# Performance work log

Measured on AMD Instinct MI355X. Metric: run time of the kernel, lower is better.

Reference implementation:

```python
import jax, jax.numpy as jnp
import numpy as np

N_NODES = 100000
N_EDGES = 1600000
EMB = 64
H1 = 128
H2 = 64


def gcn_conv(x, edge_index, W, b, num_nodes):
    # PyG GCNConv: x' = D^{-1/2}(A+I)D^{-1/2} (x W) + b, with self-loops
    x = x @ W  # [N, out]
    src, dst = edge_index[0], edge_index[1]
    loop = jnp.arange(num_nodes, dtype=src.dtype)
    src_f = jnp.concatenate([src, loop])
    dst_f = jnp.concatenate([dst, loop])
    deg = jax.ops.segment_sum(jnp.ones_like(src_f, dtype=x.dtype), dst_f,
                              num_segments=num_nodes)
    dinv = jnp.where(deg > 0, jax.lax.rsqrt(deg), 0.0)
    norm = dinv[src_f] * dinv[dst_f]           # [E+N]
    msg = x[src_f] * norm[:, None]             # gather + scale
    out = jax.ops.segment_sum(msg, dst_f, num_segments=num_nodes)
    return out + b


def setup_inputs() -> dict:
    key = jax.random.key(0)
    ks = jax.random.split(key, 12)
    category_ids = jax.random.randint(ks[0], (N_NODES,), 0, 1000)
    sub_category_ids = jax.random.randint(ks[1], (N_NODES,), 0, 5000)
    element_ids = jax.random.randint(ks[2], (N_NODES,), 0, 100000)
    edge_index = jax.random.randint(ks[3], (2, N_EDGES), 0, N_NODES)
    cat_table = jax.random.normal(ks[4], (1000, EMB), dtype=jnp.float32)
    sub_table = jax.random.normal(ks[5], (5000, EMB), dtype=jnp.float32)
    elem_table = jax.random.normal(ks[6], (100000, EMB), dtype=jnp.float32)
    W1 = jax.random.normal(ks[7], (3 * EMB, H1), dtype=jnp.float32) * (1.0 / np.sqrt(3 * EMB))
    b1 = jnp.zeros((H1,), dtype=jnp.float32)
    W2 = jax.random.normal(ks[8], (H1, H2), dtype=jnp.float32) * (1.0 / np.sqrt(H1))
    b2 = jnp.zeros((H2,), dtype=jnp.float32)
    return {
        "category_ids": category_ids,
        "sub_category_ids": sub_category_ids,
        "element_ids": element_ids,
        "edge_index": edge_index,
        "cat_table": cat_table,
        "sub_table": sub_table,
        "elem_table": elem_table,
        "W1": W1, "b1": b1, "W2": W2, "b2": b2,
    }


def reference(category_ids, sub_category_ids, element_ids, edge_index,
              cat_table, sub_table, elem_table, W1, b1, W2, b2):
    # NodeEmbedding: concat of three 64-dim lookups -> [N, 192]
    x = jnp.concatenate([cat_table[category_ids],
                         sub_table[sub_category_ids],
                         elem_table[element_ids]], axis=-1)
    x = jax.nn.relu(gcn_conv(x, edge_index, W1, b1, N_NODES))
    # dropout(0.3) is identity in eval mode
    x = jax.nn.relu(gcn_conv(x, edge_index, W2, b2, N_NODES))
    return x
```

## Files before the change

### kernel.cpp

```cpp
#include <hip/hip_runtime.h>

#define N_NODES 100000
#define EMB     64
#define H1      128
#define H2      64

#define BSHIFT  7
#define NBUCK   782
#define CAP     3072

#define OFF_DINV  0
#define OFF_ROWP  100004
#define OFF_COL   200008
#define OFF_GFILL 1800008
#define OFF_GBASE 1800792
#define OFF_SCR   1801576
#define OFF_H     4203880
#define OFF_Y     10603880
#define OFF_PCAT  17003880
#define OFF_PSUB  17131880

static __device__ __forceinline__ unsigned short f2bf(float f) {
    unsigned int u = __float_as_uint(f);
    unsigned int r = (u + 0x7fffu + ((u >> 16) & 1u)) >> 16;
    return (unsigned short)r;
}
static __device__ __forceinline__ unsigned int pack2bf(float a, float b) {
    return (unsigned int)f2bf(a) | ((unsigned int)f2bf(b) << 16);
}
static __device__ __forceinline__ float bflo(unsigned int u) {
    return __uint_as_float(u << 16);
}
static __device__ __forceinline__ float bfhi(unsigned int u) {
    return __uint_as_float(u & 0xffff0000u);
}


__global__ __launch_bounds__(256) void k_bin(
    const int* __restrict__ src, const int* __restrict__ dst, int E,
    int* __restrict__ gfill, unsigned int* __restrict__ scr)
{
    __shared__ int hist[NBUCK];
    __shared__ int basec[NBUCK];
    int t = threadIdx.x;
    for (int i = t; i < NBUCK; i += 256) hist[i] = 0;
    __syncthreads();
    int chunk = (E + gridDim.x - 1) / gridDim.x;
    int e0 = blockIdx.x * chunk;
    int e1 = min(e0 + chunk, E);
    for (int i = e0 + t; i < e1; i += 256)
        atomicAdd(&hist[dst[i] >> BSHIFT], 1);
    __syncthreads();
    for (int b = t; b < NBUCK; b += 256) {
        int c = hist[b];
        basec[b] = (c > 0) ? atomicAdd(&gfill[b], c) : 0;
        hist[b] = 0;
    }
    __syncthreads();
    for (int i = e0 + t; i < e1; i += 256) {
        int d = dst[i];
        int b = d >> BSHIFT;
        int slot = basec[b] + atomicAdd(&hist[b], 1);
        if (slot < CAP)
            scr[(size_t)b * CAP + slot] =
                ((unsigned int)(d & 127) << 17) | (unsigned int)src[i];
    }
}


__global__ __launch_bounds__(256) void k_bscan(
    const int* __restrict__ gfill, int* __restrict__ gbase,
    int* __restrict__ rowp, int E)
{
    __shared__ int sh[256];
    int t = threadIdx.x;
    int v[4]; int s = 0;
    #pragma unroll
    for (int u = 0; u < 4; ++u) {
        int i = t * 4 + u;
        v[u] = (i < NBUCK) ? gfill[i] : 0;
        s += v[u];
    }
    sh[t] = s;
    __syncthreads();
    for (int off = 1; off < 256; off <<= 1) {
        int x = (t >= off) ? sh[t - off] : 0;
        __syncthreads();
        sh[t] += x;
        __syncthreads();
    }
    int run = (t == 0) ? 0 : sh[t - 1];
    #pragma unroll
    for (int u = 0; u < 4; ++u) {
        int i = t * 4 + u;
        if (i < NBUCK) gbase[i] = run;
        run += v[u];
    }
    if (t == 255) { gbase[NBUCK] = run; rowp[N_NODES] = E; }
}


__global__ __launch_bounds__(256) void k_csr(
    const unsigned int* __restrict__ scr, const int* __restrict__ gfill,
    const int* __restrict__ gbase, int N,
    int* __restrict__ rowp, int* __restrict__ col, float* __restrict__ dinv)
{
    __shared__ unsigned int stage[CAP];
    __shared__ int hist[128];
    __shared__ int offs[128];
    __shared__ int cur[128];
    int b = blockIdx.x, t = threadIdx.x;
    int cnt = gfill[b];
    if (cnt > CAP) cnt = CAP;
    int base = gbase[b];
    if (t < 128) hist[t] = 0;
    __syncthreads();
    for (int i = t; i < cnt; i += 256) {
        unsigned int p = scr[(size_t)b * CAP + i];
        stage[i] = p;
        atomicAdd(&hist[p >> 17], 1);
    }
    __syncthreads();
    if (t < 128) offs[t] = hist[t];
    __syncthreads();
    for (int off = 1; off < 128; off <<= 1) {
        int x = 0;
        if (t < 128 && t >= off) x = offs[t - off];
        __syncthreads();
        if (t < 128) offs[t] += x;
        __syncthreads();
    }
    if (t < 128) {
        int excl = offs[t] - hist[t];
        cur[t] = 0;
        int d = b * 128 + t;
        if (d < N) {
            rowp[d] = base + excl;
            dinv[d] = rsqrtf((float)(hist[t] + 1));
        }
        offs[t] = excl;
    }
    __syncthreads();
    for (int i = t; i < cnt; i += 256) {
        unsigned int p = stage[i];
        int dl = (int)(p >> 17);
        int pos = offs[dl] + atomicAdd(&cur[dl], 1);
        col[base + pos] = (int)(p & 0x1FFFFu);
    }
}


__global__ __launch_bounds__(256) void k_ptab(
    const float* __restrict__ tab, const float* __restrict__ Wseg,
    float* __restrict__ P, int R)
{
    __shared__ float Wl[64][128];
    int t = threadIdx.x;
    for (int idx = t; idx < 64 * 128; idx += 256)
        Wl[idx >> 7][idx & 127] = Wseg[idx];
    __syncthreads();
    int cg = t & 31, ng = t >> 5;
    int r = blockIdx.x * 8 + ng;
    if (r >= R) return;
    const float* x = tab + (size_t)r * 64;
    float4 acc = make_float4(0.f, 0.f, 0.f, 0.f);
    #pragma unroll 8
    for (int k = 0; k < 64; ++k) {
        float xx = x[k];
        float4 w = *(const float4*)&Wl[k][cg * 4];
        acc.x += xx * w.x; acc.y += xx * w.y;
        acc.z += xx * w.z; acc.w += xx * w.w;
    }
    *(float4*)&P[(size_t)r * 128 + cg * 4] = acc;
}


__global__ __launch_bounds__(256) void k_gemm1(
    const int* __restrict__ cid, const int* __restrict__ sid, const int* __restrict__ eid,
    const float* __restrict__ elem_t, const float* __restrict__ W1,
    const float* __restrict__ Pcat, const float* __restrict__ Psub,
    const float* __restrict__ dinv,
    unsigned short* __restrict__ hb, int N)
{
    __shared__ float Wl[64][128];
    int t = threadIdx.x;
    const float* Wc = W1 + 128 * 128;
    for (int idx = t; idx < 64 * 128; idx += 256)
        Wl[idx >> 7][idx & 127] = Wc[idx];
    __syncthreads();

    int cg = t & 31;
    int ng = t >> 5;
    int n0 = blockIdx.x << 6;

    const float* rp[8];
    #pragma unroll
    for (int i = 0; i < 8; ++i) {
        int n = n0 + ng + 8 * i;
        int id = eid[(n < N) ? n : 0];
        rp[i] = elem_t + (size_t)id * 64;
    }
    float4 acc[8];
    #pragma unroll
    for (int i = 0; i < 8; ++i) acc[i] = make_float4(0.f, 0.f, 0.f, 0.f);

    #pragma unroll 4
    for (int k4 = 0; k4 < 16; ++k4) {
        float4 xv[8];
        #pragma unroll
        for (int i = 0; i < 8; ++i)
            xv[i] = *(const float4*)(rp[i] + k4 * 4);
        #pragma unroll
        for (int kk = 0; kk < 4; ++kk) {
            float4 w = *(const float4*)&Wl[k4 * 4 + kk][cg * 4];
            #pragma unroll
            for (int i = 0; i < 8; ++i) {
                float xx = (kk == 0) ? xv[i].x : (kk == 1) ? xv[i].y
                         : (kk == 2) ? xv[i].z : xv[i].w;
                acc[i].x += xx * w.x;
                acc[i].y += xx * w.y;
                acc[i].z += xx * w.z;
                acc[i].w += xx * w.w;
            }
        }
    }
    #pragma unroll
    for (int i = 0; i < 8; ++i) {
        int n = n0 + ng + 8 * i;
        if (n < N) {
            float4 pc = *(const float4*)&Pcat[(size_t)cid[n] * 128 + cg * 4];
            float4 ps = *(const float4*)&Psub[(size_t)sid[n] * 128 + cg * 4];
            float s = dinv[n];
            uint2 p;
            p.x = pack2bf((acc[i].x + pc.x + ps.x) * s, (acc[i].y + pc.y + ps.y) * s);
            p.y = pack2bf((acc[i].z + pc.z + ps.z) * s, (acc[i].w + pc.w + ps.w) * s);
            *(uint2*)(hb + (size_t)n * 128 + cg * 4) = p;
        }
    }
}


__global__ __launch_bounds__(256) void k_gemm2(
    const unsigned int* __restrict__ yb, const float* __restrict__ W2,
    const float* __restrict__ dinv,
    unsigned short* __restrict__ h2b, int N)
{
    __shared__ float Wl[128][64];
    int t = threadIdx.x;
    for (int idx = t; idx < 128 * 64; idx += 256)
        Wl[idx >> 6][idx & 63] = W2[idx];
    __syncthreads();

    int cg = t & 15;
    int ng = t >> 4;
    int n0 = blockIdx.x << 7;
    const unsigned int* rp[8];
    float4 acc[8];
    #pragma unroll
    for (int i = 0; i < 8; ++i) {
        acc[i] = make_float4(0.f, 0.f, 0.f, 0.f);
        int n = n0 + ng + 16 * i;
        rp[i] = yb + (size_t)((n < N) ? n : (N - 1)) * 64;
    }
    #pragma unroll 4
    for (int k4 = 0; k4 < 32; ++k4) {
        uint2 xv[8];
        #pragma unroll
        for (int i = 0; i < 8; ++i)
            xv[i] = *(const uint2*)(rp[i] + k4 * 2);
        #pragma unroll
        for (int kk = 0; kk < 4; ++kk) {
            float4 w = *(const float4*)&Wl[k4 * 4 + kk][cg * 4];
            #pragma unroll
            for (int i = 0; i < 8; ++i) {
                float xx = (kk == 0) ? bflo(xv[i].x) : (kk == 1) ? bfhi(xv[i].x)
                         : (kk == 2) ? bflo(xv[i].y) : bfhi(xv[i].y);
                acc[i].x += xx * w.x;
                acc[i].y += xx * w.y;
                acc[i].z += xx * w.z;
                acc[i].w += xx * w.w;
            }
        }
    }
    #pragma unroll
    for (int i = 0; i < 8; ++i) {
        int n = n0 + ng + 16 * i;
        if (n < N) {
            float s = dinv[n];
            uint2 p;
            p.x = pack2bf(acc[i].x * s, acc[i].y * s);
            p.y = pack2bf(acc[i].z * s, acc[i].w * s);
            *(uint2*)(h2b + (size_t)n * 64 + cg * 4) = p;
        }
    }
}


__global__ __launch_bounds__(256) void k_agg1(
    const unsigned short* __restrict__ hb, const int* __restrict__ rowp,
    const int* __restrict__ col, const float* __restrict__ dinv,
    const float* __restrict__ b1, unsigned int* __restrict__ yb, int N)
{
    int wv = threadIdx.x >> 6;
    int lane = threadIdx.x & 63;
    int d = blockIdx.x * 4 + wv;
    if (d >= N) return;
    const unsigned int* hp = (const unsigned int*)hb;
    float dd = dinv[d];
    unsigned int su = hp[(size_t)d * 64 + lane];
    float ax0 = bflo(su), ay0 = bfhi(su);
    float ax1 = 0.f, ay1 = 0.f, ax2 = 0.f, ay2 = 0.f, ax3 = 0.f, ay3 = 0.f;
    float ax4 = 0.f, ay4 = 0.f, ax5 = 0.f, ay5 = 0.f, ax6 = 0.f, ay6 = 0.f;
    float ax7 = 0.f, ay7 = 0.f;
    int e = rowp[d], e1 = rowp[d + 1];
    for (; e + 8 <= e1; e += 8) {
        int s0 = col[e + 0], s1 = col[e + 1], s2 = col[e + 2], s3 = col[e + 3];
        int s4 = col[e + 4], s5 = col[e + 5], s6 = col[e + 6], s7 = col[e + 7];
        unsigned int u0 = hp[(size_t)s0 * 64 + lane];
        unsigned int u1 = hp[(size_t)s1 * 64 + lane];
        unsigned int u2 = hp[(size_t)s2 * 64 + lane];
        unsigned int u3 = hp[(size_t)s3 * 64 + lane];
        unsigned int u4 = hp[(size_t)s4 * 64 + lane];
        unsigned int u5 = hp[(size_t)s5 * 64 + lane];
        unsigned int u6 = hp[(size_t)s6 * 64 + lane];
        unsigned int u7 = hp[(size_t)s7 * 64 + lane];
        ax0 += bflo(u0); ay0 += bfhi(u0);
        ax1 += bflo(u1); ay1 += bfhi(u1);
        ax2 += bflo(u2); ay2 += bfhi(u2);
        ax3 += bflo(u3); ay3 += bfhi(u3);
        ax4 += bflo(u4); ay4 += bfhi(u4);
        ax5 += bflo(u5); ay5 += bfhi(u5);
        ax6 += bflo(u6); ay6 += bfhi(u6);
        ax7 += bflo(u7); ay7 += bfhi(u7);
    }
    for (; e < e1; ++e) {
        unsigned int u = hp[(size_t)col[e] * 64 + lane];
        ax0 += bflo(u); ay0 += bfhi(u);
    }
    float2 bb = *(const float2*)&b1[lane * 2];
    float rx = dd * (((ax0 + ax1) + (ax2 + ax3)) + ((ax4 + ax5) + (ax6 + ax7))) + bb.x;
    float ry = dd * (((ay0 + ay1) + (ay2 + ay3)) + ((ay4 + ay5) + (ay6 + ay7))) + bb.y;
    yb[(size_t)d * 64 + lane] = pack2bf(rx > 0.f ? rx : 0.f, ry > 0.f ? ry : 0.f);
}


__global__ __launch_bounds__(256) void k_agg2(
    const unsigned short* __restrict__ h2b, const int* __restrict__ rowp,
    const int* __restrict__ col, const float* __restrict__ dinv,
    const float* __restrict__ b2, float* __restrict__ out, int N)
{
    int wv = threadIdx.x >> 6;
    int lane = threadIdx.x & 63;
    int d = blockIdx.x * 4 + wv;
    if (d >= N) return;
    float dd = dinv[d];
    float a0 = __uint_as_float((unsigned int)h2b[(size_t)d * 64 + lane] << 16);
    float a1 = 0.f, a2 = 0.f, a3 = 0.f, a4 = 0.f, a5 = 0.f, a6 = 0.f, a7 = 0.f;
    int e = rowp[d], e1 = rowp[d + 1];
    for (; e + 8 <= e1; e += 8) {
        int s0 = col[e + 0], s1 = col[e + 1], s2 = col[e + 2], s3 = col[e + 3];
        int s4 = col[e + 4], s5 = col[e + 5], s6 = col[e + 6], s7 = col[e + 7];
        a0 += __uint_as_float((unsigned int)h2b[(size_t)s0 * 64 + lane] << 16);
        a1 += __uint_as_float((unsigned int)h2b[(size_t)s1 * 64 + lane] << 16);
        a2 += __uint_as_float((unsigned int)h2b[(size_t)s2 * 64 + lane] << 16);
        a3 += __uint_as_float((unsigned int)h2b[(size_t)s3 * 64 + lane] << 16);
        a4 += __uint_as_float((unsigned int)h2b[(size_t)s4 * 64 + lane] << 16);
        a5 += __uint_as_float((unsigned int)h2b[(size_t)s5 * 64 + lane] << 16);
        a6 += __uint_as_float((unsigned int)h2b[(size_t)s6 * 64 + lane] << 16);
        a7 += __uint_as_float((unsigned int)h2b[(size_t)s7 * 64 + lane] << 16);
    }
    for (; e < e1; ++e)
        a0 += __uint_as_float((unsigned int)h2b[(size_t)col[e] * 64 + lane] << 16);
    float v = dd * (((a0 + a1) + (a2 + a3)) + ((a4 + a5) + (a6 + a7))) + b2[lane];
    out[(size_t)d * 64 + lane] = v > 0.f ? v : 0.f;
}


extern "C" void kernel_launch(void* const* d_in, const int* in_sizes, int n_in,
                              void* d_out, int out_size, void* d_ws, size_t ws_size,
                              hipStream_t stream) {
    const int*   cid    = (const int*)d_in[0];
    const int*   sid    = (const int*)d_in[1];
    const int*   eid    = (const int*)d_in[2];
    const int*   edge   = (const int*)d_in[3];
    const float* cat_t  = (const float*)d_in[4];
    const float* sub_t  = (const float*)d_in[5];
    const float* elem_t = (const float*)d_in[6];
    const float* W1     = (const float*)d_in[7];
    const float* b1     = (const float*)d_in[8];
    const float* W2     = (const float*)d_in[9];
    const float* b2     = (const float*)d_in[10];
    float* out = (float*)d_out;

    int N = in_sizes[0];
    int E = in_sizes[3] / 2;
    const int* src = edge;
    const int* dst = edge + E;

    int*   ws    = (int*)d_ws;
    float* dinv  = (float*)(ws + OFF_DINV);
    int*   rowp  = ws + OFF_ROWP;
    int*   col   = ws + OFF_COL;
    int*   gfill = ws + OFF_GFILL;
    int*   gbase = ws + OFF_GBASE;
    unsigned int* scr = (unsigned int*)(ws + OFF_SCR);
    unsigned short* hb = (unsigned short*)(ws + OFF_H);
    unsigned int*   yb = (unsigned int*)(ws + OFF_Y);
    float* Pcat = (float*)(ws + OFF_PCAT);
    float* Psub = (float*)(ws + OFF_PSUB);

    hipMemsetAsync(gfill, 0, NBUCK * sizeof(int), stream);

    k_ptab<<<125, 256, 0, stream>>>(cat_t, W1,            Pcat, 1000);
    k_ptab<<<625, 256, 0, stream>>>(sub_t, W1 + 64 * 128, Psub, 5000);

    k_bin<<<200, 256, 0, stream>>>(src, dst, E, gfill, scr);
    k_bscan<<<1, 256, 0, stream>>>(gfill, gbase, rowp, E);
    k_csr<<<NBUCK, 256, 0, stream>>>(scr, gfill, gbase, N, rowp, col, dinv);

    k_gemm1<<<(N + 63) / 64, 256, 0, stream>>>(cid, sid, eid, elem_t, W1, Pcat, Psub, dinv, hb, N);
    k_agg1<<<(N + 3) / 4, 256, 0, stream>>>(hb, rowp, col, dinv, b1, yb, N);
    k_gemm2<<<(N + 127) / 128, 256, 0, stream>>>(yb, W2, dinv, hb, N);
    k_agg2<<<(N + 3) / 4, 256, 0, stream>>>(hb, rowp, col, dinv, b2, out, N);
}
```

Measured before the change: 429.0 us.

## Process two destination nodes per wavefront in aggregation and enlarge CSR-build blocks

```diff
diff --git a/kernel.cpp b/kernel.cpp
--- a/kernel.cpp
+++ b/kernel.cpp
@@ -36,28 +36,28 @@
 }
 
 
-__global__ __launch_bounds__(256) void k_bin(
+__global__ __launch_bounds__(1024) void k_bin(
     const int* __restrict__ src, const int* __restrict__ dst, int E,
     int* __restrict__ gfill, unsigned int* __restrict__ scr)
 {
     __shared__ int hist[NBUCK];
     __shared__ int basec[NBUCK];
     int t = threadIdx.x;
-    for (int i = t; i < NBUCK; i += 256) hist[i] = 0;
+    for (int i = t; i < NBUCK; i += 1024) hist[i] = 0;
     __syncthreads();
     int chunk = (E + gridDim.x - 1) / gridDim.x;
     int e0 = blockIdx.x * chunk;
     int e1 = min(e0 + chunk, E);
-    for (int i = e0 + t; i < e1; i += 256)
+    for (int i = e0 + t; i < e1; i += 1024)
         atomicAdd(&hist[dst[i] >> BSHIFT], 1);
     __syncthreads();
-    for (int b = t; b < NBUCK; b += 256) {
+    for (int b = t; b < NBUCK; b += 1024) {
         int c = hist[b];
         basec[b] = (c > 0) ? atomicAdd(&gfill[b], c) : 0;
         hist[b] = 0;
     }
     __syncthreads();
-    for (int i = e0 + t; i < e1; i += 256) {
+    for (int i = e0 + t; i < e1; i += 1024) {
         int d = dst[i];
         int b = d >> BSHIFT;
         int slot = basec[b] + atomicAdd(&hist[b], 1);
@@ -100,7 +100,7 @@
 }
 
 
-__global__ __launch_bounds__(256) void k_csr(
+__global__ __launch_bounds__(512) void k_csr(
     const unsigned int* __restrict__ scr, const int* __restrict__ gfill,
     const int* __restrict__ gbase, int N,
     int* __restrict__ rowp, int* __restrict__ col, float* __restrict__ dinv)
@@ -115,7 +115,7 @@
     int base = gbase[b];
     if (t < 128) hist[t] = 0;
     __syncthreads();
-    for (int i = t; i < cnt; i += 256) {
+    for (int i = t; i < cnt; i += 512) {
         unsigned int p = scr[(size_t)b * CAP + i];
         stage[i] = p;
         atomicAdd(&hist[p >> 17], 1);
@@ -141,7 +141,7 @@
         offs[t] = excl;
     }
     __syncthreads();
-    for (int i = t; i < cnt; i += 256) {
+    for (int i = t; i < cnt; i += 512) {
         unsigned int p = stage[i];
         int dl = (int)(p >> 17);
         int pos = offs[dl] + atomicAdd(&cur[dl], 1);
@@ -299,80 +299,128 @@
 __global__ __launch_bounds__(256) void k_agg1(
     const unsigned short* __restrict__ hb, const int* __restrict__ rowp,
     const int* __restrict__ col, const float* __restrict__ dinv,
-    const float* __restrict__ b1, unsigned int* __restrict__ yb, int N)
-{
-    int wv = threadIdx.x >> 6;
+    const float* __restrict__ b1, unsigned int* __restrict__ yb, int N, int E)
+{
+    int w = blockIdx.x * 4 + (threadIdx.x >> 6);
     int lane = threadIdx.x & 63;
-    int d = blockIdx.x * 4 + wv;
-    if (d >= N) return;
+    int half = lane >> 5, l5 = lane & 31;
+    if (w * 2 >= N) return;
+    int d = w * 2 + half;
+    if (d >= N) d = N - 1;
     const unsigned int* hp = (const unsigned int*)hb;
     float dd = dinv[d];
-    unsigned int su = hp[(size_t)d * 64 + lane];
-    float ax0 = bflo(su), ay0 = bfhi(su);
-    float ax1 = 0.f, ay1 = 0.f, ax2 = 0.f, ay2 = 0.f, ax3 = 0.f, ay3 = 0.f;
-    float ax4 = 0.f, ay4 = 0.f, ax5 = 0.f, ay5 = 0.f, ax6 = 0.f, ay6 = 0.f;
-    float ax7 = 0.f, ay7 = 0.f;
-    int e = rowp[d], e1 = rowp[d + 1];
-    for (; e + 8 <= e1; e += 8) {
-        int s0 = col[e + 0], s1 = col[e + 1], s2 = col[e + 2], s3 = col[e + 3];
-        int s4 = col[e + 4], s5 = col[e + 5], s6 = col[e + 6], s7 = col[e + 7];
-        unsigned int u0 = hp[(size_t)s0 * 64 + lane];
-        unsigned int u1 = hp[(size_t)s1 * 64 + lane];
-        unsigned int u2 = hp[(size_t)s2 * 64 + lane];
-        unsigned int u3 = hp[(size_t)s3 * 64 + lane];
-        unsigned int u4 = hp[(size_t)s4 * 64 + lane];
-        unsigned int u5 = hp[(size_t)s5 * 64 + lane];
-        unsigned int u6 = hp[(size_t)s6 * 64 + lane];
-        unsigned int u7 = hp[(size_t)s7 * 64 + lane];
-        ax0 += bflo(u0); ay0 += bfhi(u0);
-        ax1 += bflo(u1); ay1 += bfhi(u1);
-        ax2 += bflo(u2); ay2 += bfhi(u2);
-        ax3 += bflo(u3); ay3 += bfhi(u3);
-        ax4 += bflo(u4); ay4 += bfhi(u4);
-        ax5 += bflo(u5); ay5 += bfhi(u5);
-        ax6 += bflo(u6); ay6 += bfhi(u6);
-        ax7 += bflo(u7); ay7 += bfhi(u7);
-    }
-    for (; e < e1; ++e) {
-        unsigned int u = hp[(size_t)col[e] * 64 + lane];
-        ax0 += bflo(u); ay0 += bfhi(u);
-    }
-    float2 bb = *(const float2*)&b1[lane * 2];
-    float rx = dd * (((ax0 + ax1) + (ax2 + ax3)) + ((ax4 + ax5) + (ax6 + ax7))) + bb.x;
-    float ry = dd * (((ay0 + ay1) + (ay2 + ay3)) + ((ay4 + ay5) + (ay6 + ay7))) + bb.y;
-    yb[(size_t)d * 64 + lane] = pack2bf(rx > 0.f ? rx : 0.f, ry > 0.f ? ry : 0.f);
+    uint2 su = *(const uint2*)(hp + (size_t)d * 64 + 2 * l5);
+    float a0 = bflo(su.x), a1 = bfhi(su.x), a2 = bflo(su.y), a3 = bfhi(su.y);
+    float b0_ = 0.f, b1_ = 0.f, b2_ = 0.f, b3_ = 0.f;
+    float c0_ = 0.f, c1_ = 0.f, c2_ = 0.f, c3_ = 0.f;
+    float d0_ = 0.f, d1_ = 0.f, d2_ = 0.f, d3_ = 0.f;
+    int e0 = rowp[d];
+    int len = rowp[d + 1] - e0;
+    int lo = __shfl_xor(len, 32);
+    int lm = len > lo ? len : lo;
+    int Emax = E - 1;
+    int i = 0;
+    for (; i + 8 <= lm; i += 8) {
+        int c[8];
+        #pragma unroll
+        for (int k = 0; k < 8; ++k) c[k] = col[min(e0 + i + k, Emax)];
+        #pragma unroll
+        for (int k = 0; k < 8; ++k) {
+            bool pr = (i + k) < len;
+            int idx = pr ? c[k] : d;
+            float m = pr ? 1.f : 0.f;
+            uint2 u = *(const uint2*)(hp + (size_t)idx * 64 + 2 * l5);
+            float* A = (k & 2) ? ((k & 1) ? &d0_ : &c0_) : ((k & 1) ? &b0_ : &a0);
+            A[0] += m * bflo(u.x);
+            A[1] += m * bfhi(u.x);
+            A[2] += m * bflo(u.y);
+            A[3] += m * bfhi(u.y);
+        }
+    }
+    for (; i < lm; ++i) {
+        bool pr = i < len;
+        int idx = pr ? col[min(e0 + i, Emax)] : d;
+        float m = pr ? 1.f : 0.f;
+        uint2 u = *(const uint2*)(hp + (size_t)idx * 64 + 2 * l5);
+        a0 += m * bflo(u.x); a1 += m * bfhi(u.x);
+        a2 += m * bflo(u.y); a3 += m * bfhi(u.y);
+    }
+    float4 bb = *(const float4*)&b1[l5 * 4];
+    float r0 = dd * ((a0 + b0_) + (c0_ + d0_)) + bb.x;
+    float r1 = dd * ((a1 + b1_) + (c1_ + d1_)) + bb.y;
+    float r2 = dd * ((a2 + b2_) + (c2_ + d2_)) + bb.z;
+    float r3 = dd * ((a3 + b3_) + (c3_ + d3_)) + bb.w;
+    uint2 p;
+    p.x = pack2bf(r0 > 0.f ? r0 : 0.f, r1 > 0.f ? r1 : 0.f);
+    p.y = pack2bf(r2 > 0.f ? r2 : 0.f, r3 > 0.f ? r3 : 0.f);
+    *(uint2*)(yb + (size_t)d * 64 + 2 * l5) = p;
 }
 
 
 __global__ __launch_bounds__(256) void k_agg2(
     const unsigned short* __restrict__ h2b, const int* __restrict__ rowp,
     const int* __restrict__ col, const float* __restrict__ dinv,
-    const float* __restrict__ b2, float* __restrict__ out, int N)
-{
-    int wv = threadIdx.x >> 6;
+    const float* __restrict__ b2, float* __restrict__ out, int N, int E)
+{
+    int w = blockIdx.x * 4 + (threadIdx.x >> 6);
     int lane = threadIdx.x & 63;
-    int d = blockIdx.x * 4 + wv;
-    if (d >= N) return;
+    int half = lane >> 5, l5 = lane & 31;
+    if (w * 2 >= N) return;
+    int d = w * 2 + half;
+    if (d >= N) d = N - 1;
+    const unsigned int* hp = (const unsigned int*)h2b;
     float dd = dinv[d];
-    float a0 = __uint_as_float((unsigned int)h2b[(size_t)d * 64 + lane] << 16);
-    float a1 = 0.f, a2 = 0.f, a3 = 0.f, a4 = 0.f, a5 = 0.f, a6 = 0.f, a7 = 0.f;
-    int e = rowp[d], e1 = rowp[d + 1];
-    for (; e + 8 <= e1; e += 8) {
-        int s0 = col[e + 0], s1 = col[e + 1], s2 = col[e + 2], s3 = col[e + 3];
-        int s4 = col[e + 4], s5 = col[e + 5], s6 = col[e + 6], s7 = col[e + 7];
-        a0 += __uint_as_float((unsigned int)h2b[(size_t)s0 * 64 + lane] << 16);
-        a1 += __uint_as_float((unsigned int)h2b[(size_t)s1 * 64 + lane] << 16);
-        a2 += __uint_as_float((unsigned int)h2b[(size_t)s2 * 64 + lane] << 16);
-        a3 += __uint_as_float((unsigned int)h2b[(size_t)s3 * 64 + lane] << 16);
-        a4 += __uint_as_float((unsigned int)h2b[(size_t)s4 * 64 + lane] << 16);
-        a5 += __uint_as_float((unsigned int)h2b[(size_t)s5 * 64 + lane] << 16);
-        a6 += __uint_as_float((unsigned int)h2b[(size_t)s6 * 64 + lane] << 16);
-        a7 += __uint_as_float((unsigned int)h2b[(size_t)s7 * 64 + lane] << 16);
-    }
-    for (; e < e1; ++e)
-        a0 += __uint_as_float((unsigned int)h2b[(size_t)col[e] * 64 + lane] << 16);
-    float v = dd * (((a0 + a1) + (a2 + a3)) + ((a4 + a5) + (a6 + a7))) + b2[lane];
-    out[(size_t)d * 64 + lane] = v > 0.f ? v : 0.f;
+    unsigned int su = hp[(size_t)d * 32 + l5];
+    float a0 = bflo(su), a1 = bfhi(su);
+    float b0_ = 0.f, b1_ = 0.f, c0_ = 0.f, c1_ = 0.f, d0_ = 0.f, d1_ = 0.f;
+    float e0_ = 0.f, e1_ = 0.f, f0_ = 0.f, f1_ = 0.f, g0_ = 0.f, g1_ = 0.f;
+    float h0_ = 0.f, h1_ = 0.f;
+    int e0 = rowp[d];
+    int len = rowp[d + 1] - e0;
+    int lo = __shfl_xor(len, 32);
+    int lm = len > lo ? len : lo;
+    int Emax = E - 1;
+    int i = 0;
+    for (; i + 8 <= lm; i += 8) {
+        int c[8];
+        #pragma unroll
+        for (int k = 0; k < 8; ++k) c[k] = col[min(e0 + i + k, Emax)];
+        unsigned int u[8];
+        #pragma unroll
+        for (int k = 0; k < 8; ++k) {
+            int idx = ((i + k) < len) ? c[k] : d;
+            u[k] = hp[(size_t)idx * 32 + l5];
+        }
+        #pragma unroll
+        for (int k = 0; k < 8; ++k) {
+            float m = ((i + k) < len) ? 1.f : 0.f;
+            float vx = m * bflo(u[k]), vy = m * bfhi(u[k]);
+            switch (k) {
+                case 0: a0 += vx; a1 += vy; break;
+                case 1: b0_ += vx; b1_ += vy; break;
+                case 2: c0_ += vx; c1_ += vy; break;
+                case 3: d0_ += vx; d1_ += vy; break;
+                case 4: e0_ += vx; e1_ += vy; break;
+                case 5: f0_ += vx; f1_ += vy; break;
+                case 6: g0_ += vx; g1_ += vy; break;
+                default: h0_ += vx; h1_ += vy; break;
+            }
+        }
+    }
+    for (; i < lm; ++i) {
+        bool pr = i < len;
+        int idx = pr ? col[min(e0 + i, Emax)] : d;
+        float m = pr ? 1.f : 0.f;
+        unsigned int u = hp[(size_t)idx * 32 + l5];
+        a0 += m * bflo(u); a1 += m * bfhi(u);
+    }
+    float2 bb = *(const float2*)&b2[l5 * 2];
+    float v0 = dd * (((a0 + b0_) + (c0_ + d0_)) + ((e0_ + f0_) + (g0_ + h0_))) + bb.x;
+    float v1 = dd * (((a1 + b1_) + (c1_ + d1_)) + ((e1_ + f1_) + (g1_ + h1_))) + bb.y;
+    float2 r;
+    r.x = v0 > 0.f ? v0 : 0.f;
+    r.y = v1 > 0.f ? v1 : 0.f;
+    *(float2*)&out[(size_t)d * 64 + 2 * l5] = r;
 }
 
 
@@ -414,12 +462,13 @@
     k_ptab<<<125, 256, 0, stream>>>(cat_t, W1,            Pcat, 1000);
     k_ptab<<<625, 256, 0, stream>>>(sub_t, W1 + 64 * 128, Psub, 5000);
 
-    k_bin<<<200, 256, 0, stream>>>(src, dst, E, gfill, scr);
+    k_bin<<<200, 1024, 0, stream>>>(src, dst, E, gfill, scr);
     k_bscan<<<1, 256, 0, stream>>>(gfill, gbase, rowp, E);
-    k_csr<<<NBUCK, 256, 0, stream>>>(scr, gfill, gbase, N, rowp, col, dinv);
+    k_csr<<<NBUCK, 512, 0, stream>>>(scr, gfill, gbase, N, rowp, col, dinv);
 
     k_gemm1<<<(N + 63) / 64, 256, 0, stream>>>(cid, sid, eid, elem_t, W1, Pcat, Psub, dinv, hb, N);
-    k_agg1<<<(N + 3) / 4, 256, 0, stream>>>(hb, rowp, col, dinv, b1, yb, N);
+    int aggblk = (N / 2 + 3) / 4;
+    k_agg1<<<aggblk, 256, 0, stream>>>(hb, rowp, col, dinv, b1, yb, N, E);
     k_gemm2<<<(N + 127) / 128, 256, 0, stream>>>(yb, W2, dinv, hb, N);
-    k_agg2<<<(N + 3) / 4, 256, 0, stream>>>(hb, rowp, col, dinv, b2, out, N);
-}
+    k_agg2<<<aggblk, 256, 0, stream>>>(hb, rowp, col, dinv, b2, out, N, E);
+}
```

Result: no change. 421.4 us (-1.8%).
